# Kernel optimization log

Hardware: AMD Instinct MI355X
Metric: run time of the kernel (lower is better)

The kernel has to match this reference:

```python
import jax, jax.numpy as jnp
import numpy as np

B, S, NDIMS, NHEADS, NPOS = 1, 2048, 1024, 16, 64
PER_HEAD = NDIMS // NHEADS


def setup_inputs() -> dict:
    key = jax.random.key(0)
    ks = jax.random.split(key, 9)
    sc = 1.0 / np.sqrt(NDIMS)
    inp = {
        'q': jax.random.normal(ks[0], (B, S, NDIMS), jnp.float32),
        'k': jax.random.normal(ks[1], (B, S, NDIMS), jnp.float32),
        'v': jax.random.normal(ks[2], (B, S, NDIMS), jnp.float32),
        'Wq_w': jax.random.normal(ks[3], (NDIMS, NDIMS), jnp.float32) * sc,
        'Wq_b': jnp.zeros((NDIMS,), jnp.float32),
        'Wk_w': jax.random.normal(ks[4], (NDIMS, NDIMS), jnp.float32) * sc,
        'Wk_b': jnp.zeros((NDIMS,), jnp.float32),
        'Wv_w': jax.random.normal(ks[5], (NDIMS, NDIMS), jnp.float32) * sc,
        'Wv_b': jnp.zeros((NDIMS,), jnp.float32),
        'Wo_w': jax.random.normal(ks[6], (NDIMS, NDIMS), jnp.float32) * sc,
        'Wo_b': jnp.zeros((NDIMS,), jnp.float32),
        'pos_emb': jax.random.normal(ks[7], (PER_HEAD, NPOS), jnp.float32) * 0.02,
        'nheads': NHEADS,
    }
    return inp


def cope(query, attn_logits, pos_emb):
    # query: [b,h,q,d]; attn_logits: [b,h,q,k]; pos_emb: [d,npos]
    npos_max = pos_emb.shape[-1]
    gates = jax.nn.sigmoid(attn_logits)
    # reverse cumsum over key axis: flip -> cumsum -> flip
    pos = jnp.flip(jnp.cumsum(jnp.flip(gates, axis=-1), axis=-1), axis=-1)
    pos = jnp.minimum(pos, npos_max - 1)
    pos_ceil = jnp.ceil(pos).astype(jnp.int32)
    pos_floor = jnp.floor(pos).astype(jnp.int32)
    logits_int = jnp.einsum('bhqd,dn->bhqn', query, pos_emb)  # [b,h,q,npos]
    logits_ceil = jnp.take_along_axis(logits_int, pos_ceil, axis=-1)
    logits_floor = jnp.take_along_axis(logits_int, pos_floor, axis=-1)
    w = pos - pos_floor
    return logits_ceil * w + logits_floor * (1.0 - w)


def reference(q, k, v, Wq_w, Wq_b, Wk_w, Wk_b, Wv_w, Wv_b, Wo_w, Wo_b, pos_emb, nheads):
    b, s, ndims = q.shape
    d = ndims // nheads
    def heads(x, W, bb):
        y = x @ W.T + bb
        return y.reshape(b, s, nheads, d).transpose(0, 2, 1, 3)  # [b,h,s,d]
    Q = heads(q, Wq_w, Wq_b)
    K = heads(k, Wk_w, Wk_b)
    V = heads(v, Wv_w, Wv_b)
    logits = jnp.einsum('bhqd,bhkd->bhqk', Q, K) / jnp.sqrt(jnp.asarray(d, Q.dtype))
    scores = jax.nn.softmax(logits + cope(Q, logits, pos_emb), axis=-1)
    out = jnp.einsum('bhqk,bhkd->bhqd', scores, V)
    out = out.transpose(0, 2, 1, 3).reshape(b, s, ndims)
    return out @ Wo_w.T + Wo_b
```

## Files before the change

kernel.cpp:

```cpp
#include <hip/hip_runtime.h>
#include <hip/hip_bf16.h>
#include <math.h>

#define SEQ 2048
#define ND  1024
#define NH  16
#define HD  64
#define NPOSN 64

typedef short short8 __attribute__((ext_vector_type(8)));
typedef short short4v __attribute__((ext_vector_type(4)));
typedef float floatx4 __attribute__((ext_vector_type(4)));

#define MFMA16(A, B, C) __builtin_amdgcn_mfma_f32_16x16x32_bf16((A), (B), (C), 0, 0, 0)

#define ASYNC16(gp, lp)                                                                     \
  __builtin_amdgcn_global_load_lds((const __attribute__((address_space(1))) unsigned int*)(gp), \
                                   (__attribute__((address_space(3))) unsigned int*)(lp), 16, 0, 0)

__device__ __forceinline__ short f2bf(float x) {
  __hip_bfloat16 h = __float2bfloat16(x);
  return *reinterpret_cast<short*>(&h);
}
__device__ __forceinline__ float bf2f(short s) {
  __hip_bfloat16 h = *reinterpret_cast<__hip_bfloat16*>(&s);
  return __bfloat162float(h);
}
__device__ __forceinline__ float lane_bcast(float v, int l) {
  return __int_as_float(__builtin_amdgcn_readlane(__float_as_int(v), l));
}

struct Prep2 {
  const float* x0; short* x0h; short* x0l;
  const float* x1; short* x1h; short* x1l;
  const float* x2; short* x2h; short* x2l;
  const float* w0; short* w0h; short* w0l;
  const float* w1; short* w1h; short* w1l;
  const float* w2; short* w2h; short* w2l;
  const float* w3; short* w3h; short* w3l;
  const float* pe; short* peT;
};

__device__ __forceinline__ void split_planes(const float* __restrict__ in,
                                             short* __restrict__ oh,
                                             short* __restrict__ ol) {
  int r = blockIdx.x;
  int c = threadIdx.x << 2;
  float4 v = *(const float4*)(in + (size_t)r * 1024 + c);
  short4v hi, lo;
  hi.x = f2bf(v.x); lo.x = f2bf(v.x - bf2f(hi.x));
  hi.y = f2bf(v.y); lo.y = f2bf(v.y - bf2f(hi.y));
  hi.z = f2bf(v.z); lo.z = f2bf(v.z - bf2f(hi.z));
  hi.w = f2bf(v.w); lo.w = f2bf(v.w - bf2f(hi.w));
  *(short4v*)(oh + (size_t)r * 1024 + c) = hi;
  *(short4v*)(ol + (size_t)r * 1024 + c) = lo;
}

__global__ __launch_bounds__(256)
void prep2(Prep2 P) {
  const int z = blockIdx.z;
  if (z < 3) {
    const float* in = (z == 0) ? P.x0 : (z == 1 ? P.x1 : P.x2);
    short* oh = (z == 0) ? P.x0h : (z == 1 ? P.x1h : P.x2h);
    short* ol = (z == 0) ? P.x0l : (z == 1 ? P.x1l : P.x2l);
    split_planes(in, oh, ol);
  } else if (z < 7) {
    if (blockIdx.x >= 1024) return;
    const float* in = (z == 3) ? P.w0 : (z == 4 ? P.w1 : (z == 5 ? P.w2 : P.w3));
    short* oh = (z == 3) ? P.w0h : (z == 4 ? P.w1h : (z == 5 ? P.w2h : P.w3h));
    short* ol = (z == 3) ? P.w0l : (z == 4 ? P.w1l : (z == 5 ? P.w2l : P.w3l));
    split_planes(in, oh, ol);
  } else {
    if (blockIdx.x != 0) return;
    for (int i = threadIdx.x; i < 4096; i += 256) {
      int n = i >> 6, d = i & 63;
      P.peT[n * 64 + d] = f2bf(P.pe[d * 64 + n]);
    }
  }
}

struct GArg2 {
  const short* Ahi; const short* Alo;
  const short* Bhi; const short* Blo;
  const float* bias;
  void* o0; void* o1; int mode;
};

__device__ __forceinline__ void gemm_store(const GArg2& A, int m, int n, float v) {
  if (A.mode == 0) {
    ((float*)A.o0)[(size_t)m * 1024 + n] = v;
  } else {
    const short hi = f2bf(v);
    const int hh = n >> 6, d = n & 63;
    const size_t off = (A.mode == 1) ? ((size_t)(hh * SEQ + m) * 64 + d)
                                     : ((size_t)(hh * 64 + d) * SEQ + m);
    ((short*)A.o0)[off] = hi;
    if (A.o1) {
      const short lo = f2bf(v - bf2f(hi));
      ((short*)A.o1)[off] = lo;
    }
  }
}

__global__ __launch_bounds__(256, 3)
void gemm_planes(GArg2 ga, GArg2 gb, GArg2 gc) {
  __shared__ __align__(16) short Ah[8192];
  __shared__ __align__(16) short Al[8192];
  __shared__ __align__(16) short Bh[4096];
  __shared__ __align__(16) short Bl[4096];
  GArg2 A = (blockIdx.z == 0) ? ga : ((blockIdx.z == 1) ? gb : gc);
  const bool t3 = (A.Blo != nullptr);
  const int t = threadIdx.x;
  const int w = t >> 6, lane = t & 63;
  const int col = lane & 15, quad = lane >> 4;
  const int m0 = blockIdx.x * 128, n0 = blockIdx.y * 64;
  const int wr = (w & 1) * 64, wc = (w >> 1) * 32;
  const int lrow8 = lane >> 3;
  const int src_c = (lane & 7) ^ lrow8;

  floatx4 acc[4][2] = {};
  for (int kk = 0; kk < 1024; kk += 64) {
#pragma unroll
    for (int i = 0; i < 4; ++i) {
      const int inst = 4 * w + i;
      const int row = inst * 8 + lrow8;
      ASYNC16(A.Ahi + (size_t)(m0 + row) * 1024 + kk + src_c * 8, &Ah[inst * 512]);
      ASYNC16(A.Alo + (size_t)(m0 + row) * 1024 + kk + src_c * 8, &Al[inst * 512]);
    }
#pragma unroll
    for (int i = 0; i < 2; ++i) {
      const int inst = 2 * w + i;
      const int row = inst * 8 + lrow8;
      ASYNC16(A.Bhi + (size_t)(n0 + row) * 1024 + kk + src_c * 8, &Bh[inst * 512]);
      if (t3) ASYNC16(A.Blo + (size_t)(n0 + row) * 1024 + kk + src_c * 8, &Bl[inst * 512]);
    }
    __syncthreads();
#pragma unroll
    for (int ks = 0; ks < 2; ++ks) {
      short8 ah[4], al[4], bh[2], bl[2];
#pragma unroll
      for (int mt = 0; mt < 4; ++mt) {
        const int row = wr + mt * 16 + col;
        const int pos = ((ks * 4 + quad) ^ (row & 7)) * 8;
        ah[mt] = *(const short8*)&Ah[row * 64 + pos];
        al[mt] = *(const short8*)&Al[row * 64 + pos];
      }
#pragma unroll
      for (int nt = 0; nt < 2; ++nt) {
        const int row = wc + nt * 16 + col;
        const int pos = ((ks * 4 + quad) ^ (row & 7)) * 8;
        bh[nt] = *(const short8*)&Bh[row * 64 + pos];
        if (t3) bl[nt] = *(const short8*)&Bl[row * 64 + pos];
      }
#pragma unroll
      for (int mt = 0; mt < 4; ++mt)
#pragma unroll
        for (int nt = 0; nt < 2; ++nt) {
          acc[mt][nt] = MFMA16(ah[mt], bh[nt], acc[mt][nt]);
          acc[mt][nt] = MFMA16(al[mt], bh[nt], acc[mt][nt]);
          if (t3) acc[mt][nt] = MFMA16(ah[mt], bl[nt], acc[mt][nt]);
        }
    }
    __syncthreads();
  }
#pragma unroll
  for (int nt = 0; nt < 2; ++nt) {
    const int n = n0 + wc + nt * 16 + col;
    const float bb = A.bias[n];
#pragma unroll
    for (int mt = 0; mt < 4; ++mt)
#pragma unroll
      for (int r = 0; r < 4; ++r)
        gemm_store(A, m0 + wr + mt * 16 + quad * 4 + r, n, acc[mt][nt][r] + bb);
  }
}

__global__ __launch_bounds__(256, 3)
void gemm_planes64(GArg2 A) {
  __shared__ __align__(16) short Ah[4096];
  __shared__ __align__(16) short Al[4096];
  __shared__ __align__(16) short Bh[4096];
  __shared__ __align__(16) short Bl[4096];
  const bool t3 = (A.Blo != nullptr);
  const int t = threadIdx.x;
  const int w = t >> 6, lane = t & 63;
  const int col = lane & 15, quad = lane >> 4;
  const int m0 = blockIdx.x * 64, n0 = blockIdx.y * 64;
  const int wr = (w & 1) * 32, wc = (w >> 1) * 32;
  const int lrow8 = lane >> 3;
  const int src_c = (lane & 7) ^ lrow8;

  floatx4 acc[2][2] = {};
  for (int kk = 0; kk < 1024; kk += 64) {
#pragma unroll
    for (int i = 0; i < 2; ++i) {
      const int inst = 2 * w + i;
      const int row = inst * 8 + lrow8;
      ASYNC16(A.Ahi + (size_t)(m0 + row) * 1024 + kk + src_c * 8, &Ah[inst * 512]);
      ASYNC16(A.Alo + (size_t)(m0 + row) * 1024 + kk + src_c * 8, &Al[inst * 512]);
      ASYNC16(A.Bhi + (size_t)(n0 + row) * 1024 + kk + src_c * 8, &Bh[inst * 512]);
      if (t3) ASYNC16(A.Blo + (size_t)(n0 + row) * 1024 + kk + src_c * 8, &Bl[inst * 512]);
    }
    __syncthreads();
#pragma unroll
    for (int ks = 0; ks < 2; ++ks) {
      short8 ah[2], al[2], bh[2], bl[2];
#pragma unroll
      for (int mt = 0; mt < 2; ++mt) {
        const int row = wr + mt * 16 + col;
        const int pos = ((ks * 4 + quad) ^ (row & 7)) * 8;
        ah[mt] = *(const short8*)&Ah[row * 64 + pos];
        al[mt] = *(const short8*)&Al[row * 64 + pos];
      }
#pragma unroll
      for (int nt = 0; nt < 2; ++nt) {
        const int row = wc + nt * 16 + col;
        const int pos = ((ks * 4 + quad) ^ (row & 7)) * 8;
        bh[nt] = *(const short8*)&Bh[row * 64 + pos];
        if (t3) bl[nt] = *(const short8*)&Bl[row * 64 + pos];
      }
#pragma unroll
      for (int mt = 0; mt < 2; ++mt)
#pragma unroll
        for (int nt = 0; nt < 2; ++nt) {
          acc[mt][nt] = MFMA16(ah[mt], bh[nt], acc[mt][nt]);
          acc[mt][nt] = MFMA16(al[mt], bh[nt], acc[mt][nt]);
          if (t3) acc[mt][nt] = MFMA16(ah[mt], bl[nt], acc[mt][nt]);
        }
    }
    __syncthreads();
  }
#pragma unroll
  for (int nt = 0; nt < 2; ++nt) {
    const int n = n0 + wc + nt * 16 + col;
    const float bb = A.bias[n];
#pragma unroll
    for (int mt = 0; mt < 2; ++mt)
#pragma unroll
      for (int r = 0; r < 4; ++r)
        gemm_store(A, m0 + wr + mt * 16 + quad * 4 + r, n, acc[mt][nt][r] + bb);
  }
}

__global__ __launch_bounds__(256, 2)
void cope_attn_mfma(const short* __restrict__ Qhi, const short* __restrict__ Qlo,
                    const short* __restrict__ Khi, const short* __restrict__ Vthi,
                    const short* __restrict__ peT,
                    short* __restrict__ AOhi, short* __restrict__ AOlo) {
  __shared__ __align__(16) short Klds[2][4096];
  __shared__ __align__(16) short Vlds[2][4096];
  __shared__ __align__(16) short Phi[4][16][72];
  __shared__ float2 lis2[4][16][65];
  const int tid = threadIdx.x;
  const int w = tid >> 6, lane = tid & 63;
  const int col = lane & 15, quad = lane >> 4;
  const int h = blockIdx.x & 15;
  const int q0 = (blockIdx.x >> 4) * 64 + w * 16;

  const short* Kb = Khi + (size_t)h * SEQ * 64;
  const short* Vb = Vthi + (size_t)h * 64 * SEQ;

  const int lrow8 = lane >> 3;
  const int src_c = (lane & 7) ^ lrow8;

  auto stage = [&](int kt, int buf) {
#pragma unroll
    for (int i = 0; i < 2; ++i) {
      const int inst = 2 * w + i;
      const int row = inst * 8 + lrow8;
      ASYNC16(Kb + (size_t)(kt * 64 + row) * 64 + src_c * 8, &Klds[buf][inst * 512]);
      ASYNC16(Vb + (size_t)row * SEQ + kt * 64 + src_c * 8, &Vlds[buf][inst * 512]);
    }
  };

  short8 qB[2][2];
#pragma unroll
  for (int ks = 0; ks < 2; ++ks) {
    qB[ks][0] = *(const short8*)(Qhi + (size_t)(h * SEQ + q0 + col) * 64 + ks * 32 + quad * 8);
    qB[ks][1] = *(const short8*)(Qlo + (size_t)(h * SEQ + q0 + col) * 64 + ks * 32 + quad * 8);
  }

  stage(31, 0);

  {
    floatx4 li[4] = {};
#pragma unroll
    for (int nt = 0; nt < 4; ++nt)
#pragma unroll
      for (int ks = 0; ks < 2; ++ks) {
        short8 pb = *(const short8*)(peT + (nt * 16 + col) * 64 + ks * 32 + quad * 8);
        li[nt] = MFMA16(qB[ks][0], pb, li[nt]);
        li[nt] = MFMA16(qB[ks][1], pb, li[nt]);
      }
#pragma unroll
    for (int nt = 0; nt < 4; ++nt)
#pragma unroll
      for (int r = 0; r < 4; ++r) {
        const int qr = quad * 4 + r;
        const int pos = nt * 16 + col;
        const float v = li[nt][r];
        lis2[w][qr][pos].x = v;
        if (pos > 0) lis2[w][qr][pos - 1].y = v;
        if (pos == 63) lis2[w][qr][63].y = v;
      }
  }
  __syncthreads();
  const float lis63 = lis2[w][col][63].x;

  float lrow = 0.f;
  float carry = 0.f;
  bool fast = false;
  floatx4 O[4] = {};

  const int swz = col & 7;

#pragma unroll 1
  for (int it = 0; it < 32; ++it) {
    const int kt = 31 - it;
    const int buf = it & 1;
    if (kt > 0) stage(kt - 1, buf ^ 1);

    short8 kf[4][2], vf[2][4];
#pragma unroll
    for (int ksub = 0; ksub < 4; ++ksub)
#pragma unroll
      for (int ks = 0; ks < 2; ++ks)
        kf[ksub][ks] =
            *(const short8*)&Klds[buf][(ksub * 16 + col) * 64 + (((ks * 4 + quad) ^ swz) * 8)];
#pragma unroll
    for (int ks = 0; ks < 2; ++ks)
#pragma unroll
      for (int dt = 0; dt < 4; ++dt)
        vf[ks][dt] =
            *(const short8*)&Vlds[buf][(dt * 16 + col) * 64 + (((ks * 4 + quad) ^ swz) * 8)];

    floatx4 S[4] = {};
#pragma unroll
    for (int ksub = 0; ksub < 4; ++ksub)
#pragma unroll
      for (int ks = 0; ks < 2; ++ks) {
        S[ksub] = MFMA16(kf[ksub][ks], qB[ks][0], S[ksub]);
        S[ksub] = MFMA16(kf[ksub][ks], qB[ks][1], S[ksub]);
      }
    float sv[4][4];
#pragma unroll
    for (int ksub = 0; ksub < 4; ++ksub)
#pragma unroll
      for (int r = 0; r < 4; ++r) sv[ksub][r] = S[ksub][r] * 0.125f;

    if (!fast && __all((int)(carry >= 63.0f))) fast = true;

    float p4[4][4];
    if (fast) {
#pragma unroll
      for (int ksub = 0; ksub < 4; ++ksub)
#pragma unroll
        for (int r = 0; r < 4; ++r) {
          float pr = __expf(sv[ksub][r] + lis63);
          p4[ksub][r] = pr;
          lrow += pr;
        }
    } else {
      float g[4][4];
#pragma unroll
      for (int ksub = 0; ksub < 4; ++ksub)
#pragma unroll
        for (int r = 0; r < 4; ++r)
          g[ksub][r] = __builtin_amdgcn_rcpf(1.0f + __expf(-sv[ksub][r]));
      float l[4][4], S4[4];
#pragma unroll
      for (int ksub = 0; ksub < 4; ++ksub) {
        l[ksub][3] = g[ksub][3];
        l[ksub][2] = l[ksub][3] + g[ksub][2];
        l[ksub][1] = l[ksub][2] + g[ksub][1];
        l[ksub][0] = l[ksub][1] + g[ksub][0];
        S4[ksub] = l[ksub][0];
      }
      float Sq[4], T[4];
#pragma unroll
      for (int ksub = 0; ksub < 4; ++ksub) {
        float d16 = __shfl_down(S4[ksub], 16, 64);
        float d32 = __shfl_down(S4[ksub], 32, 64);
        float d48 = __shfl_down(S4[ksub], 48, 64);
        float u16 = __shfl_up(S4[ksub], 16, 64);
        float u32 = __shfl_up(S4[ksub], 32, 64);
        float u48 = __shfl_up(S4[ksub], 48, 64);
        float sq = ((quad < 3) ? d16 : 0.f) + ((quad < 2) ? d32 : 0.f) + ((quad < 1) ? d48 : 0.f);
        float pq = ((quad > 0) ? u16 : 0.f) + ((quad > 1) ? u32 : 0.f) + ((quad > 2) ? u48 : 0.f);
        Sq[ksub] = sq;
        T[ksub] = pq + S4[ksub] + sq;
      }
      float U[4];
      U[3] = carry;
      U[2] = U[3] + T[3];
      U[1] = U[2] + T[2];
      U[0] = U[1] + T[1];
      carry = U[0] + T[0];
#pragma unroll
      for (int ksub = 0; ksub < 4; ++ksub)
#pragma unroll
        for (int r = 0; r < 4; ++r) {
          float p = fminf(U[ksub] + Sq[ksub] + l[ksub][r], 63.0f);
          float pf = floorf(p);
          int fi = (int)pf;
          float wq = p - pf;
          float2 lfc = lis2[w][col][fi];
          float pr = __expf(sv[ksub][r] + lfc.x + wq * (lfc.y - lfc.x));
          p4[ksub][r] = pr;
          lrow += pr;
        }
    }
#pragma unroll
    for (int ksub = 0; ksub < 4; ++ksub)
#pragma unroll
      for (int rp = 0; rp < 2; ++rp) {
        short h0 = f2bf(p4[ksub][2 * rp]);
        short h1 = f2bf(p4[ksub][2 * rp + 1]);
        *(int*)&Phi[w][col][ksub * 16 + quad * 4 + 2 * rp] =
            (unsigned short)h0 | ((unsigned)(unsigned short)h1 << 16);
      }
    short8 pa[2];
#pragma unroll
    for (int ks = 0; ks < 2; ++ks)
      pa[ks] = *(const short8*)&Phi[w][col][ks * 32 + quad * 8];
#pragma unroll
    for (int ks = 0; ks < 2; ++ks)
#pragma unroll
      for (int dt = 0; dt < 4; ++dt)
        O[dt] = MFMA16(pa[ks], vf[ks][dt], O[dt]);

    __syncthreads();
  }

  float lr = lrow;
  lr += __shfl_xor(lr, 16, 64);
  lr += __shfl_xor(lr, 32, 64);
  float inv[4];
#pragma unroll
  for (int r = 0; r < 4; ++r) inv[r] = 1.0f / __shfl(lr, quad * 4 + r, 64);
#pragma unroll
  for (int dt = 0; dt < 4; ++dt)
#pragma unroll
    for (int r = 0; r < 4; ++r) {
      float val = O[dt][r] * inv[r];
      int q = q0 + quad * 4 + r;
      int cg = h * 64 + dt * 16 + col;
      short hi = f2bf(val), lo = f2bf(val - bf2f(hi));
      AOhi[(size_t)q * 1024 + cg] = hi;
      AOlo[(size_t)q * 1024 + cg] = lo;
    }
}

template <int MODE>
__global__ __launch_bounds__(256)
void gemm_bt_f32(const float* __restrict__ X, const float* __restrict__ W,
                 const float* __restrict__ bias, float* __restrict__ C,
                 int M, int N, int K) {
  __shared__ __align__(16) float Xs[16][68];
  __shared__ __align__(16) float Ws[16][68];
  const int t = threadIdx.x;
  const int tx = t & 15, ty = t >> 4;
  const int m0 = blockIdx.x * 64, n0 = blockIdx.y * 64;
  const int r = t >> 2;
  const int c4 = (t & 3) << 2;
  const float* Xp = X + (size_t)(m0 + r) * K + c4;
  const float* Wp = W + (size_t)(n0 + r) * K + c4;
  float acc[4][4] = {};
  for (int k0 = 0; k0 < K; k0 += 16) {
    float4 xv = *(const float4*)(Xp + k0);
    float4 wv = *(const float4*)(Wp + k0);
    __syncthreads();
    Xs[c4 + 0][r] = xv.x; Xs[c4 + 1][r] = xv.y; Xs[c4 + 2][r] = xv.z; Xs[c4 + 3][r] = xv.w;
    Ws[c4 + 0][r] = wv.x; Ws[c4 + 1][r] = wv.y; Ws[c4 + 2][r] = wv.z; Ws[c4 + 3][r] = wv.w;
    __syncthreads();
#pragma unroll
    for (int k = 0; k < 16; ++k) {
      const float4 xr = *(const float4*)&Xs[k][ty << 2];
      const float4 wr = *(const float4*)&Ws[k][tx << 2];
      const float xa[4] = {xr.x, xr.y, xr.z, xr.w};
      const float wa[4] = {wr.x, wr.y, wr.z, wr.w};
#pragma unroll
      for (int i = 0; i < 4; ++i)
#pragma unroll
        for (int j = 0; j < 4; ++j) acc[i][j] += xa[i] * wa[j];
    }
  }
#pragma unroll
  for (int i = 0; i < 4; ++i) {
    const int m = m0 + (ty << 2) + i;
#pragma unroll
    for (int j = 0; j < 4; ++j) {
      const int n = n0 + (tx << 2) + j;
      const float v = acc[i][j] + bias[n];
      if (MODE == 0) C[(size_t)m * N + n] = v;
      else { const int hh = n >> 6, d = n & 63; C[((size_t)hh * SEQ + m) * HD + d] = v; }
    }
  }
}

__global__ __launch_bounds__(256)
void cope_attn_f32(const float* __restrict__ Qh, const float* __restrict__ Kh,
                   const float* __restrict__ Vh, const float* __restrict__ pe,
                   float* __restrict__ AO) {
  __shared__ float Kt[64][65];
  __shared__ float Vt[64][65];
  __shared__ float lis[16][64];
  const int t = threadIdx.x;
  const int lane = t & 63;
  const int w = t >> 6;
  const int h = blockIdx.y;
  const int qbase = blockIdx.x * 16 + w * 4;
  float qreg[4];
#pragma unroll
  for (int rr = 0; rr < 4; ++rr)
    qreg[rr] = Qh[((size_t)h * SEQ + qbase + rr) * HD + lane];
  float li[4] = {0.f, 0.f, 0.f, 0.f};
  for (int d = 0; d < 64; ++d) {
    const float pv = pe[d * NPOSN + lane];
#pragma unroll
    for (int rr = 0; rr < 4; ++rr) li[rr] += lane_bcast(qreg[rr], d) * pv;
  }
#pragma unroll
  for (int rr = 0; rr < 4; ++rr) lis[w * 4 + rr][lane] = li[rr];
  float mrow[4] = {-1e30f, -1e30f, -1e30f, -1e30f};
  float lrow[4] = {0.f, 0.f, 0.f, 0.f};
  float carry[4] = {0.f, 0.f, 0.f, 0.f};
  float acc[4] = {0.f, 0.f, 0.f, 0.f};
  for (int kt = (SEQ / 64) - 1; kt >= 0; --kt) {
    const int k0 = kt * 64;
    __syncthreads();
#pragma unroll
    for (int i = 0; i < 4; ++i) {
      const int lin = t + i * 256;
      const int row = lin >> 4, cc = (lin & 15) << 2;
      const float4 kv = *(const float4*)(Kh + ((size_t)h * SEQ + k0 + row) * HD + cc);
      Kt[row][cc + 0] = kv.x; Kt[row][cc + 1] = kv.y; Kt[row][cc + 2] = kv.z; Kt[row][cc + 3] = kv.w;
      const float4 vv = *(const float4*)(Vh + ((size_t)h * SEQ + k0 + row) * HD + cc);
      Vt[row][cc + 0] = vv.x; Vt[row][cc + 1] = vv.y; Vt[row][cc + 2] = vv.z; Vt[row][cc + 3] = vv.w;
    }
    __syncthreads();
    float svv[4] = {0.f, 0.f, 0.f, 0.f};
#pragma unroll
    for (int d = 0; d < 64; ++d) {
      const float kd = Kt[lane][d];
#pragma unroll
      for (int rr = 0; rr < 4; ++rr) svv[rr] += lane_bcast(qreg[rr], d) * kd;
    }
    float p4[4], scl[4];
#pragma unroll
    for (int rr = 0; rr < 4; ++rr) {
      const float s = svv[rr] * 0.125f;
      const float gg = 1.0f / (1.0f + __expf(-s));
      float gs = gg;
#pragma unroll
      for (int off = 1; off < 64; off <<= 1) {
        const float tt = __shfl_down(gs, off, 64);
        gs += (lane + off < 64) ? tt : 0.0f;
      }
      const float tot = lane_bcast(gs, 0);
      float p = carry[rr] + gs;
      carry[rr] += tot;
      p = fminf(p, 63.0f);
      const float pf = floorf(p);
      const float wq = p - pf;
      const int fi = (int)pf;
      const int ci = (int)ceilf(p);
      const float cope = lis[w * 4 + rr][ci] * wq + lis[w * 4 + rr][fi] * (1.0f - wq);
      const float av = s + cope;
      float mt = av;
#pragma unroll
      for (int off = 32; off > 0; off >>= 1) mt = fmaxf(mt, __shfl_xor(mt, off, 64));
      const float nm = fmaxf(mrow[rr], mt);
      const float sc = __expf(mrow[rr] - nm);
      const float p2 = __expf(av - nm);
      float psum = p2;
#pragma unroll
      for (int off = 32; off > 0; off >>= 1) psum += __shfl_xor(psum, off, 64);
      lrow[rr] = lrow[rr] * sc + psum;
      mrow[rr] = nm;
      p4[rr] = p2;
      scl[rr] = sc;
    }
#pragma unroll
    for (int rr = 0; rr < 4; ++rr) acc[rr] *= scl[rr];
#pragma unroll
    for (int j = 0; j < 64; ++j) {
      const float vj = Vt[j][lane];
#pragma unroll
      for (int rr = 0; rr < 4; ++rr) acc[rr] += lane_bcast(p4[rr], j) * vj;
    }
  }
#pragma unroll
  for (int rr = 0; rr < 4; ++rr)
    AO[(size_t)(qbase + rr) * ND + h * HD + lane] = acc[rr] / lrow[rr];
}

extern "C" void kernel_launch(void* const* d_in, const int* in_sizes, int n_in,
                              void* d_out, int out_size, void* d_ws, size_t ws_size,
                              hipStream_t stream) {
  (void)in_sizes; (void)n_in; (void)out_size;
  const float* q    = (const float*)d_in[0];
  const float* k    = (const float*)d_in[1];
  const float* v    = (const float*)d_in[2];
  const float* Wq_w = (const float*)d_in[3];
  const float* Wq_b = (const float*)d_in[4];
  const float* Wk_w = (const float*)d_in[5];
  const float* Wk_b = (const float*)d_in[6];
  const float* Wv_w = (const float*)d_in[7];
  const float* Wv_b = (const float*)d_in[8];
  const float* Wo_w = (const float*)d_in[9];
  const float* Wo_b = (const float*)d_in[10];
  const float* pe   = (const float*)d_in[11];
  float* out = (float*)d_out;
  char* ws = (char*)d_ws;

  const size_t XP = (size_t)SEQ * 1024 * 2;
  const size_t WP = (size_t)1024 * 1024 * 2;
  const size_t HB = (size_t)SEQ * 1024 * 2;
  const size_t NEED = 6 * XP + 8 * WP + 4 * HB + 8192;

  if (ws_size >= NEED) {
    short* Xqh = (short*)ws;               short* Xql = (short*)(ws + XP);
    short* Xkh = (short*)(ws + 2 * XP);    short* Xkl = (short*)(ws + 3 * XP);
    short* Xvh = (short*)(ws + 4 * XP);    short* Xvl = (short*)(ws + 5 * XP);
    char*  wb  = ws + 6 * XP;
    short* Wqh = (short*)wb;               short* Wql = (short*)(wb + WP);
    short* Wkh = (short*)(wb + 2 * WP);    short* Wkl = (short*)(wb + 3 * WP);
    short* Wvh = (short*)(wb + 4 * WP);    short* Wvl = (short*)(wb + 5 * WP);
    short* Woh = (short*)(wb + 6 * WP);    short* Wol = (short*)(wb + 7 * WP);
    char*  hb  = wb + 8 * WP;
    short* Qhi = (short*)hb;               short* Qlo = (short*)(hb + HB);
    short* Khi = (short*)(hb + 2 * HB);    short* Vthi = (short*)(hb + 3 * HB);
    short* peT = (short*)(hb + 4 * HB);
    short* AOhi = Xqh;
    short* AOlo = Xql;

    Prep2 P{q, Xqh, Xql, k, Xkh, Xkl, v, Xvh, Xvl,
            Wq_w, Wqh, Wql, Wk_w, Wkh, Wkl, Wv_w, Wvh, Wvl, Wo_w, Woh, Wol,
            pe, peT};
    prep2<<<dim3(2048, 1, 8), 256, 0, stream>>>(P);
    GArg2 aq{Xqh, Xql, Wqh, Wql, Wq_b, Qhi, Qlo, 1};
    GArg2 ak{Xkh, Xkl, Wkh, nullptr, Wk_b, Khi, nullptr, 1};
    GArg2 av{Xvh, Xvl, Wvh, nullptr, Wv_b, Vthi, nullptr, 2};
    gemm_planes<<<dim3(16, 16, 3), 256, 0, stream>>>(aq, ak, av);
    cope_attn_mfma<<<512, 256, 0, stream>>>(Qhi, Qlo, Khi, Vthi, peT, AOhi, AOlo);
    GArg2 ao{AOhi, AOlo, Woh, Wol, Wo_b, (void*)out, nullptr, 0};
    gemm_planes64<<<dim3(32, 16), 256, 0, stream>>>(ao);
  } else {
    const size_t per = (size_t)NH * SEQ * HD;
    float* Qh = (float*)d_ws;
    float* Kh = Qh + per;
    float* Vh = Kh + per;
    float* AO = Vh + per;
    dim3 gblk(256), ggrd(SEQ / 64, ND / 64);
    gemm_bt_f32<1><<<ggrd, gblk, 0, stream>>>(q, Wq_w, Wq_b, Qh, SEQ, ND, ND);
    gemm_bt_f32<1><<<ggrd, gblk, 0, stream>>>(k, Wk_w, Wk_b, Kh, SEQ, ND, ND);
    gemm_bt_f32<1><<<ggrd, gblk, 0, stream>>>(v, Wv_w, Wv_b, Vh, SEQ, ND, ND);
    cope_attn_f32<<<dim3(SEQ / 16, NH), 256, 0, stream>>>(Qh, Kh, Vh, pe, AO);
    gemm_bt_f32<0><<<ggrd, gblk, 0, stream>>>(AO, Wo_w, Wo_b, out, SEQ, ND, ND);
  }
}
```

Baseline: 203.0 us.

## Drop low-precision bf16 planes for QKV projections and load V directly from global

The Q/K/V projection GEMMs now use only the high bf16 plane of the inputs and weights. This removes the lo-plane prep writes, the lo-plane async loads, and the extra MFMAs that compensated for bf16 rounding. The output projection still uses split planes. In the attention kernel, V tiles are no longer staged through LDS; each lane reads its V fragments straight from global memory. The changes cut prep, GEMM compute and LDS traffic, but they lower the accuracy of Q/K/V, and the direct V reads may be less coalesced.

```diff
diff --git a/kernel.cpp b/kernel.cpp
--- a/kernel.cpp
+++ b/kernel.cpp
@@ -31,19 +31,19 @@
 }
 
 struct Prep2 {
-  const float* x0; short* x0h; short* x0l;
-  const float* x1; short* x1h; short* x1l;
-  const float* x2; short* x2h; short* x2l;
-  const float* w0; short* w0h; short* w0l;
-  const float* w1; short* w1h; short* w1l;
-  const float* w2; short* w2h; short* w2l;
+  const float* x0; short* x0h;
+  const float* x1; short* x1h;
+  const float* x2; short* x2h;
+  const float* w0; short* w0h;
+  const float* w1; short* w1h;
+  const float* w2; short* w2h;
   const float* w3; short* w3h; short* w3l;
   const float* pe; short* peT;
 };
 
 __device__ __forceinline__ void split_planes(const float* __restrict__ in,
                                              short* __restrict__ oh,
-                                             short* __restrict__ ol) {
+                                             short* __restrict__ ol, bool wlo) {
   int r = blockIdx.x;
   int c = threadIdx.x << 2;
   float4 v = *(const float4*)(in + (size_t)r * 1024 + c);
@@ -53,7 +53,7 @@
   hi.z = f2bf(v.z); lo.z = f2bf(v.z - bf2f(hi.z));
   hi.w = f2bf(v.w); lo.w = f2bf(v.w - bf2f(hi.w));
   *(short4v*)(oh + (size_t)r * 1024 + c) = hi;
-  *(short4v*)(ol + (size_t)r * 1024 + c) = lo;
+  if (wlo) *(short4v*)(ol + (size_t)r * 1024 + c) = lo;
 }
 
 __global__ __launch_bounds__(256)
@@ -62,14 +62,15 @@
   if (z < 3) {
     const float* in = (z == 0) ? P.x0 : (z == 1 ? P.x1 : P.x2);
     short* oh = (z == 0) ? P.x0h : (z == 1 ? P.x1h : P.x2h);
-    short* ol = (z == 0) ? P.x0l : (z == 1 ? P.x1l : P.x2l);
-    split_planes(in, oh, ol);
-  } else if (z < 7) {
+    split_planes(in, oh, nullptr, false);
+  } else if (z < 6) {
     if (blockIdx.x >= 1024) return;
-    const float* in = (z == 3) ? P.w0 : (z == 4 ? P.w1 : (z == 5 ? P.w2 : P.w3));
-    short* oh = (z == 3) ? P.w0h : (z == 4 ? P.w1h : (z == 5 ? P.w2h : P.w3h));
-    short* ol = (z == 3) ? P.w0l : (z == 4 ? P.w1l : (z == 5 ? P.w2l : P.w3l));
-    split_planes(in, oh, ol);
+    const float* in = (z == 3) ? P.w0 : (z == 4 ? P.w1 : P.w2);
+    short* oh = (z == 3) ? P.w0h : (z == 4 ? P.w1h : P.w2h);
+    split_planes(in, oh, nullptr, false);
+  } else if (z == 6) {
+    if (blockIdx.x >= 1024) return;
+    split_planes(P.w3, P.w3h, P.w3l, true);
   } else {
     if (blockIdx.x != 0) return;
     for (int i = threadIdx.x; i < 4096; i += 256) {
@@ -109,6 +110,7 @@
   __shared__ __align__(16) short Bh[4096];
   __shared__ __align__(16) short Bl[4096];
   GArg2 A = (blockIdx.z == 0) ? ga : ((blockIdx.z == 1) ? gb : gc);
+  const bool a2 = (A.Alo != nullptr);
   const bool t3 = (A.Blo != nullptr);
   const int t = threadIdx.x;
   const int w = t >> 6, lane = t & 63;
@@ -125,7 +127,7 @@
       const int inst = 4 * w + i;
       const int row = inst * 8 + lrow8;
       ASYNC16(A.Ahi + (size_t)(m0 + row) * 1024 + kk + src_c * 8, &Ah[inst * 512]);
-      ASYNC16(A.Alo + (size_t)(m0 + row) * 1024 + kk + src_c * 8, &Al[inst * 512]);
+      if (a2) ASYNC16(A.Alo + (size_t)(m0 + row) * 1024 + kk + src_c * 8, &Al[inst * 512]);
     }
 #pragma unroll
     for (int i = 0; i < 2; ++i) {
@@ -143,7 +145,7 @@
         const int row = wr + mt * 16 + col;
         const int pos = ((ks * 4 + quad) ^ (row & 7)) * 8;
         ah[mt] = *(const short8*)&Ah[row * 64 + pos];
-        al[mt] = *(const short8*)&Al[row * 64 + pos];
+        if (a2) al[mt] = *(const short8*)&Al[row * 64 + pos];
       }
 #pragma unroll
       for (int nt = 0; nt < 2; ++nt) {
@@ -157,7 +159,7 @@
 #pragma unroll
         for (int nt = 0; nt < 2; ++nt) {
           acc[mt][nt] = MFMA16(ah[mt], bh[nt], acc[mt][nt]);
-          acc[mt][nt] = MFMA16(al[mt], bh[nt], acc[mt][nt]);
+          if (a2) acc[mt][nt] = MFMA16(al[mt], bh[nt], acc[mt][nt]);
           if (t3) acc[mt][nt] = MFMA16(ah[mt], bl[nt], acc[mt][nt]);
         }
     }
@@ -248,7 +250,6 @@
                     const short* __restrict__ peT,
                     short* __restrict__ AOhi, short* __restrict__ AOlo) {
   __shared__ __align__(16) short Klds[2][4096];
-  __shared__ __align__(16) short Vlds[2][4096];
   __shared__ __align__(16) short Phi[4][16][72];
   __shared__ float2 lis2[4][16][65];
   const int tid = threadIdx.x;
@@ -269,7 +270,6 @@
       const int inst = 2 * w + i;
       const int row = inst * 8 + lrow8;
       ASYNC16(Kb + (size_t)(kt * 64 + row) * 64 + src_c * 8, &Klds[buf][inst * 512]);
-      ASYNC16(Vb + (size_t)row * SEQ + kt * 64 + src_c * 8, &Vlds[buf][inst * 512]);
     }
   };
 
@@ -320,19 +320,21 @@
     const int buf = it & 1;
     if (kt > 0) stage(kt - 1, buf ^ 1);
 
-    short8 kf[4][2], vf[2][4];
+    short8 vf[2][4];
+#pragma unroll
+    for (int ks = 0; ks < 2; ++ks)
+#pragma unroll
+      for (int dt = 0; dt < 4; ++dt)
+        vf[ks][dt] = *(const short8*)(Vb + (size_t)(dt * 16 + col) * SEQ +
+                                      kt * 64 + ks * 32 + quad * 8);
+
+    short8 kf[4][2];
 #pragma unroll
     for (int ksub = 0; ksub < 4; ++ksub)
 #pragma unroll
       for (int ks = 0; ks < 2; ++ks)
         kf[ksub][ks] =
             *(const short8*)&Klds[buf][(ksub * 16 + col) * 64 + (((ks * 4 + quad) ^ swz) * 8)];
-#pragma unroll
-    for (int ks = 0; ks < 2; ++ks)
-#pragma unroll
-      for (int dt = 0; dt < 4; ++dt)
-        vf[ks][dt] =
-            *(const short8*)&Vlds[buf][(dt * 16 + col) * 64 + (((ks * 4 + quad) ^ swz) * 8)];
 
     floatx4 S[4] = {};
 #pragma unroll
@@ -621,12 +623,12 @@
 
   if (ws_size >= NEED) {
     short* Xqh = (short*)ws;               short* Xql = (short*)(ws + XP);
-    short* Xkh = (short*)(ws + 2 * XP);    short* Xkl = (short*)(ws + 3 * XP);
-    short* Xvh = (short*)(ws + 4 * XP);    short* Xvl = (short*)(ws + 5 * XP);
+    short* Xkh = (short*)(ws + 2 * XP);
+    short* Xvh = (short*)(ws + 4 * XP);
     char*  wb  = ws + 6 * XP;
-    short* Wqh = (short*)wb;               short* Wql = (short*)(wb + WP);
-    short* Wkh = (short*)(wb + 2 * WP);    short* Wkl = (short*)(wb + 3 * WP);
-    short* Wvh = (short*)(wb + 4 * WP);    short* Wvl = (short*)(wb + 5 * WP);
+    short* Wqh = (short*)wb;
+    short* Wkh = (short*)(wb + 2 * WP);
+    short* Wvh = (short*)(wb + 4 * WP);
     short* Woh = (short*)(wb + 6 * WP);    short* Wol = (short*)(wb + 7 * WP);
     char*  hb  = wb + 8 * WP;
     short* Qhi = (short*)hb;               short* Qlo = (short*)(hb + HB);
@@ -635,13 +637,12 @@
     short* AOhi = Xqh;
     short* AOlo = Xql;
 
-    Prep2 P{q, Xqh, Xql, k, Xkh, Xkl, v, Xvh, Xvl,
-            Wq_w, Wqh, Wql, Wk_w, Wkh, Wkl, Wv_w, Wvh, Wvl, Wo_w, Woh, Wol,
-            pe, peT};
+    Prep2 P{q, Xqh, k, Xkh, v, Xvh, Wq_w, Wqh, Wk_w, Wkh, Wv_w, Wvh,
+            Wo_w, Woh, Wol, pe, peT};
     prep2<<<dim3(2048, 1, 8), 256, 0, stream>>>(P);
-    GArg2 aq{Xqh, Xql, Wqh, Wql, Wq_b, Qhi, Qlo, 1};
-    GArg2 ak{Xkh, Xkl, Wkh, nullptr, Wk_b, Khi, nullptr, 1};
-    GArg2 av{Xvh, Xvl, Wvh, nullptr, Wv_b, Vthi, nullptr, 2};
+    GArg2 aq{Xqh, nullptr, Wqh, nullptr, Wq_b, Qhi, Qlo, 1};
+    GArg2 ak{Xkh, nullptr, Wkh, nullptr, Wk_b, Khi, nullptr, 1};
+    GArg2 av{Xvh, nullptr, Wvh, nullptr, Wv_b, Vthi, nullptr, 2};
     gemm_planes<<<dim3(16, 16, 3), 256, 0, stream>>>(aq, ak, av);
     cope_attn_mfma<<<512, 256, 0, stream>>>(Qhi, Qlo, Khi, Vthi, peT, AOhi, AOlo);
     GArg2 ao{AOhi, AOlo, Woh, Wol, Wo_b, (void*)out, nullptr, 0};
```

New measurement: 228.1 us. +12.3%, slower.
